# Kernel optimization log

Measured on AMD Instinct MI355X. Metric: run time of the kernel, lower is better.

Reference implementation:

```python
import jax, jax.numpy as jnp
import numpy as np

S = 3072        # packed sequence length
DIM = 1280      # hidden size
H = 16          # num heads
HD = DIM // H   # head dim = 80
NSEG = 3        # number of packed segments


def setup_inputs() -> dict:
    key = jax.random.key(0)
    ks = jax.random.split(key, 6)
    hidden_states = jax.random.normal(ks[0], (S, DIM), jnp.float32)
    cos = jax.random.uniform(ks[1], (S, HD), jnp.float32, minval=-1.0, maxval=1.0)
    sin = jax.random.uniform(ks[2], (S, HD), jnp.float32, minval=-1.0, maxval=1.0)
    qkv_w = jax.random.normal(ks[3], (3 * DIM, DIM), jnp.float32) * 0.02
    qkv_b = jnp.zeros((3 * DIM,), jnp.float32)
    proj_w = jax.random.normal(ks[4], (DIM, DIM), jnp.float32) * 0.02
    proj_b = jnp.zeros((DIM,), jnp.float32)
    # 3 equal segments; cu_seqlens = [0, 1024, 2048, 3072]
    cu_seqlens = jnp.arange(NSEG + 1, dtype=jnp.int32) * (S // NSEG)
    return {
        "hidden_states": hidden_states, "cos": cos, "sin": sin,
        "qkv_w": qkv_w, "qkv_b": qkv_b, "proj_w": proj_w, "proj_b": proj_b,
        "cu_seqlens": cu_seqlens,
    }


def rotate_half(x):
    x1, x2 = jnp.split(x, 2, axis=-1)
    return jnp.concatenate((-x2, x1), axis=-1)


def reference(hidden_states, cos, sin, qkv_w, qkv_b, proj_w, proj_b, cu_seqlens):
    seq = hidden_states.shape[0]
    # QKV projection: [S, 3*DIM] -> [S, 3, H, HD]
    qkv = (hidden_states @ qkv_w.T + qkv_b).reshape(seq, 3, H, HD)
    q, k, v = qkv[:, 0], qkv[:, 1], qkv[:, 2]  # each [S, H, HD]
    # RoPE in float32, cos/sin broadcast over heads via [S, 1, HD]
    c = cos[:, None, :].astype(jnp.float32)
    s = sin[:, None, :].astype(jnp.float32)
    qf, kf = q.astype(jnp.float32), k.astype(jnp.float32)
    q = (qf * c + rotate_half(qf) * s).astype(q.dtype)
    k = (kf * c + rotate_half(kf) * s).astype(k.dtype)
    # Block-diagonal additive mask from cu_seqlens (vectorized, no loop)
    pos = jnp.arange(seq)
    seg = jnp.searchsorted(cu_seqlens, pos, side="right")  # segment id per token
    neg = jnp.finfo(jnp.float32).min
    mask = jnp.where(seg[:, None] == seg[None, :], 0.0, neg)  # [S, S]
    # Dense attention over packed sequence
    scores = jnp.einsum("shd,thd->hst", q, k) / np.sqrt(HD).astype(np.float32)
    scores = scores + mask  # broadcast over heads
    attn = jax.nn.softmax(scores.astype(jnp.float32), axis=-1).astype(q.dtype)
    out = jnp.einsum("hst,thd->shd", attn, v).reshape(seq, DIM)
    return out @ proj_w.T + proj_b
```

## Files before the change

### kernel.cpp

```cpp
#include <hip/hip_runtime.h>
#include <hip/hip_bf16.h>


#define S_TOT 3072
#define DIM   1280
#define NH    16
#define HD    80
#define SEG   1024
#define TDIM  3840

typedef short v8s __attribute__((ext_vector_type(8)));
typedef float v4f __attribute__((ext_vector_type(4)));

__device__ __forceinline__ short f2bf(float v) {
  __hip_bfloat16 b = __float2bfloat16(v);
  return *reinterpret_cast<short*>(&b);
}

__device__ __forceinline__ float bf2f(short s) {
  unsigned u = ((unsigned)(unsigned short)s) << 16;
  float f;
  __builtin_memcpy(&f, &u, 4);
  return f;
}

#define CVT_N1 (S_TOT * DIM / 4)
#define CVT_N2 (TDIM * DIM / 4)
#define CVT_N3 (DIM * DIM / 4)
__global__ __launch_bounds__(256) void cvt3(const float* __restrict__ in1,
                                            const float* __restrict__ in2,
                                            const float* __restrict__ in3,
                                            __hip_bfloat16* __restrict__ o1,
                                            __hip_bfloat16* __restrict__ o2,
                                            __hip_bfloat16* __restrict__ o3) {
  int i = blockIdx.x * 256 + threadIdx.x;
  const float* in;
  __hip_bfloat16* out;
  if (i < CVT_N1) { in = in1; out = o1; }
  else if (i < CVT_N1 + CVT_N2) { in = in2; out = o2; i -= CVT_N1; }
  else { in = in3; out = o3; i -= CVT_N1 + CVT_N2; }
  const float4 v = ((const float4*)in)[i];
  __hip_bfloat162 p0, p1;
  p0.x = __float2bfloat16(v.x); p0.y = __float2bfloat16(v.y);
  p1.x = __float2bfloat16(v.z); p1.y = __float2bfloat16(v.w);
  __hip_bfloat162* o = (__hip_bfloat162*)(out + (size_t)i * 4);
  o[0] = p0; o[1] = p1;
}

__global__ __launch_bounds__(256) void gemm1_c(const __hip_bfloat16* __restrict__ A,
                                               const __hip_bfloat16* __restrict__ B,
                                               const float* __restrict__ bias,
                                               __hip_bfloat16* __restrict__ C,
                                               int M, int N, int K) {
  __shared__ __align__(16) short Abuf[2][8192];
  __shared__ __align__(16) short Bbuf[2][8192];
  const int tid  = threadIdx.x;
  const int wave = tid >> 6;
  const int lane = tid & 63;
  const int quad = lane >> 4;
  const int l16  = lane & 15;
  const int bm = blockIdx.x * 128;
  const int bn = blockIdx.y * 128;
  const int wm = (wave >> 1) * 64;
  const int wn = (wave & 1) * 64;

  const int srow = tid >> 3;
  const int skh  = tid & 7;
  const __hip_bfloat16* Ag[4];
  const __hip_bfloat16* Bg[4];
  int So[4];
  #pragma unroll
  for (int l = 0; l < 4; ++l) {
    const int row = l * 32 + srow;
    Ag[l] = A + (size_t)(bm + row) * K + skh * 8;
    Bg[l] = B + (size_t)(bn + row) * K + skh * 8;
    So[l] = (row * 8 + (skh ^ (row & 7))) * 8;
  }

  v4f acc[4][4];
  const v4f vz = {0.f, 0.f, 0.f, 0.f};
  #pragma unroll
  for (int i = 0; i < 4; ++i)
    #pragma unroll
    for (int j = 0; j < 4; ++j) acc[i][j] = vz;

  const int sw = l16 & 7;
  const int nk = K >> 6;
  v8s ra[4], rb[4];

  #pragma unroll
  for (int l = 0; l < 4; ++l) { ra[l] = *(const v8s*)Ag[l]; rb[l] = *(const v8s*)Bg[l]; }
  #pragma unroll
  for (int l = 0; l < 4; ++l) {
    *(v8s*)&Abuf[0][So[l]] = ra[l];
    *(v8s*)&Bbuf[0][So[l]] = rb[l];
  }
  __syncthreads();

  for (int k = 0; k < nk; ++k) {
    const int cur = k & 1;
    const bool more = (k + 1 < nk);
    if (more) {
      const int off = (k + 1) * 64;
      #pragma unroll
      for (int l = 0; l < 4; ++l) {
        ra[l] = *(const v8s*)(Ag[l] + off);
        rb[l] = *(const v8s*)(Bg[l] + off);
      }
    }
    #pragma unroll
    for (int s = 0; s < 2; ++s) {
      const int khx = (s * 4 + quad) ^ sw;
      v8s af[4], bf[4];
      #pragma unroll
      for (int i = 0; i < 4; ++i) {
        af[i] = *(const v8s*)&Abuf[cur][((wm + i * 16 + l16) * 8 + khx) * 8];
        bf[i] = *(const v8s*)&Bbuf[cur][((wn + i * 16 + l16) * 8 + khx) * 8];
      }
      #pragma unroll
      for (int i = 0; i < 4; ++i)
        #pragma unroll
        for (int j = 0; j < 4; ++j)
          acc[i][j] = __builtin_amdgcn_mfma_f32_16x16x32_bf16(af[i], bf[j], acc[i][j], 0, 0, 0);
    }
    if (more) {
      #pragma unroll
      for (int l = 0; l < 4; ++l) {
        *(v8s*)&Abuf[1 - cur][So[l]] = ra[l];
        *(v8s*)&Bbuf[1 - cur][So[l]] = rb[l];
      }
    }
    __syncthreads();
  }

  #pragma unroll
  for (int j = 0; j < 4; ++j) {
    const int col = bn + wn + j * 16 + l16;
    const float bj = bias[col];
    #pragma unroll
    for (int i = 0; i < 4; ++i) {
      const int row0 = bm + wm + i * 16 + quad * 4;
      #pragma unroll
      for (int r = 0; r < 4; ++r)
        C[(size_t)(row0 + r) * N + col] = __float2bfloat16(acc[i][j][r] + bj);
    }
  }
}

__global__ __launch_bounds__(256) void gemm2_c(const __hip_bfloat16* __restrict__ A,
                                               const __hip_bfloat16* __restrict__ B,
                                               const float* __restrict__ bias,
                                               float* __restrict__ C,
                                               int M, int N, int K) {
  __shared__ __align__(16) short Abuf[2][4096];
  __shared__ __align__(16) short Bbuf[2][8192];
  const int tid  = threadIdx.x;
  const int wave = tid >> 6;
  const int lane = tid & 63;
  const int quad = lane >> 4;
  const int l16  = lane & 15;
  const int bm = blockIdx.x * 64;
  const int bn = blockIdx.y * 128;
  const int wm = (wave & 1) * 32;
  const int wn = (wave >> 1) * 64;

  const int srow = tid >> 3;
  const int skh  = tid & 7;
  const __hip_bfloat16* Ag[2];
  const __hip_bfloat16* Bg[4];
  int Ao[2], Bo[4];
  #pragma unroll
  for (int l = 0; l < 2; ++l) {
    const int row = l * 32 + srow;
    Ag[l] = A + (size_t)(bm + row) * K + skh * 8;
    Ao[l] = (row * 8 + (skh ^ (row & 7))) * 8;
  }
  #pragma unroll
  for (int l = 0; l < 4; ++l) {
    const int row = l * 32 + srow;
    Bg[l] = B + (size_t)(bn + row) * K + skh * 8;
    Bo[l] = (row * 8 + (skh ^ (row & 7))) * 8;
  }

  v4f acc[2][4];
  const v4f vz = {0.f, 0.f, 0.f, 0.f};
  #pragma unroll
  for (int i = 0; i < 2; ++i)
    #pragma unroll
    for (int j = 0; j < 4; ++j) acc[i][j] = vz;

  const int sw = l16 & 7;
  const int nk = K >> 6;
  v8s ra[2], rb[4];

  #pragma unroll
  for (int l = 0; l < 2; ++l) ra[l] = *(const v8s*)Ag[l];
  #pragma unroll
  for (int l = 0; l < 4; ++l) rb[l] = *(const v8s*)Bg[l];
  #pragma unroll
  for (int l = 0; l < 2; ++l) *(v8s*)&Abuf[0][Ao[l]] = ra[l];
  #pragma unroll
  for (int l = 0; l < 4; ++l) *(v8s*)&Bbuf[0][Bo[l]] = rb[l];
  __syncthreads();

  for (int k = 0; k < nk; ++k) {
    const int cur = k & 1;
    const bool more = (k + 1 < nk);
    if (more) {
      const int off = (k + 1) * 64;
      #pragma unroll
      for (int l = 0; l < 2; ++l) ra[l] = *(const v8s*)(Ag[l] + off);
      #pragma unroll
      for (int l = 0; l < 4; ++l) rb[l] = *(const v8s*)(Bg[l] + off);
    }
    #pragma unroll
    for (int s = 0; s < 2; ++s) {
      const int khx = (s * 4 + quad) ^ sw;
      v8s af[2], bf[4];
      #pragma unroll
      for (int i = 0; i < 2; ++i)
        af[i] = *(const v8s*)&Abuf[cur][((wm + i * 16 + l16) * 8 + khx) * 8];
      #pragma unroll
      for (int j = 0; j < 4; ++j)
        bf[j] = *(const v8s*)&Bbuf[cur][((wn + j * 16 + l16) * 8 + khx) * 8];
      #pragma unroll
      for (int i = 0; i < 2; ++i)
        #pragma unroll
        for (int j = 0; j < 4; ++j)
          acc[i][j] = __builtin_amdgcn_mfma_f32_16x16x32_bf16(af[i], bf[j], acc[i][j], 0, 0, 0);
    }
    if (more) {
      #pragma unroll
      for (int l = 0; l < 2; ++l) *(v8s*)&Abuf[1 - cur][Ao[l]] = ra[l];
      #pragma unroll
      for (int l = 0; l < 4; ++l) *(v8s*)&Bbuf[1 - cur][Bo[l]] = rb[l];
    }
    __syncthreads();
  }

  #pragma unroll
  for (int j = 0; j < 4; ++j) {
    const int col = bn + wn + j * 16 + l16;
    const float bj = bias[col];
    #pragma unroll
    for (int i = 0; i < 2; ++i) {
      const int row0 = bm + wm + i * 16 + quad * 4;
      #pragma unroll
      for (int r = 0; r < 4; ++r)
        C[(size_t)(row0 + r) * N + col] = acc[i][j][r] + bj;
    }
  }
}

#define QK_BLOCKS ((2 * S_TOT * 16 * 12) / 256)
#define V_BLOCKS  ((3 * 16 * 16 * 8 * 96) / 256)
__global__ __launch_bounds__(256) void pack_all(const __hip_bfloat16* __restrict__ qkv,
                                                const float* __restrict__ cos_,
                                                const float* __restrict__ sin_,
                                                short* __restrict__ Qp,
                                                short* __restrict__ Kp,
                                                short* __restrict__ Vp) {
  const int bid = blockIdx.x;
  if (bid < QK_BLOCKS) {
    const int idx = bid * 256 + threadIdx.x;
    const int kd = idx % 12;
    const int h  = (idx / 12) % 16;
    const int s  = (idx / 192) % S_TOT;
    const int p  = idx / (192 * S_TOT);
    const int seg = s >> 10, tb = (s >> 6) & 15, t = s & 63;
    short* out = (p ? Kp : Qp) +
                 ((size_t)(((seg * 16 + h) * 16 + tb) * 12 + kd) * 64 + t) * 8;
    short tmp[8];
    if (kd >= 10) {
      #pragma unroll
      for (int j = 0; j < 8; ++j) tmp[j] = 0;
      *(int4*)out = *(int4*)tmp;
      return;
    }
    const short* row = (const short*)qkv + (size_t)s * TDIM + p * DIM + h * HD;
    const int d0 = kd * 8;
    const v8s xm = *(const v8s*)(row + d0);
    const v8s xr = *(const v8s*)(row + d0 + ((kd < 5) ? 40 : -40));
    const float sgn = (kd < 5) ? -1.f : 1.f;
    const float scale = (p == 0) ? 0.111803398874989485f : 1.0f;
    #pragma unroll
    for (int j = 0; j < 8; ++j) {
      const int d = d0 + j;
      const float v = (bf2f(xm[j]) * cos_[s * HD + d] +
                       sgn * bf2f(xr[j]) * sin_[s * HD + d]) * scale;
      tmp[j] = f2bf(v);
    }
    *(int4*)out = *(int4*)tmp;
  } else {
    const int idx = (bid - QK_BLOCKS) * 256 + threadIdx.x;
    const int d  = idx % 96;
    const int td = (idx / 96) % 8;
    const int tb = (idx / 768) % 16;
    const int h  = (idx / (768 * 16)) % 16;
    const int seg = idx / (768 * 256);
    const int s0 = seg * SEG + tb * 64 + td * 8;
    const short* q = (const short*)qkv;
    short tmp[8];
    if (d < 80) {
      #pragma unroll
      for (int j = 0; j < 8; ++j)
        tmp[j] = q[(size_t)(s0 + j) * TDIM + 2 * DIM + h * HD + d];
    } else {
      const short fill = (d == 80) ? (short)0x3F80 : (short)0;
      #pragma unroll
      for (int j = 0; j < 8; ++j) tmp[j] = fill;
    }
    *(int4*)(Vp + (size_t)idx * 8) = *(int4*)tmp;
  }
}

__global__ __launch_bounds__(256, 4) void attn_mfma(const short* __restrict__ Qp,
                                                    const short* __restrict__ Kp,
                                                    const short* __restrict__ Vp,
                                                    __hip_bfloat16* __restrict__ out) {
  __shared__ __align__(16) short Ks[64 * 96];
  __shared__ __align__(16) short Vs[64 * 96];
  __shared__ __align__(16) short Ps[4][16 * 68];

  const int qt  = blockIdx.x;
  const int h   = blockIdx.y;
  const int seg = blockIdx.z;
  const int tid  = threadIdx.x;
  const int wave = tid >> 6;
  const int lane = tid & 63;
  const int quad = lane >> 4;
  const int l16  = lane & 15;
  const int sh16 = seg * 16 + h;

  const short* Qg = Qp + (size_t)(sh16 * 16 + qt) * 6144;
  const short* Kg = Kp + (size_t)sh16 * 16 * 6144;
  const short* Vg = Vp + (size_t)sh16 * 16 * 6144;

  v8s af[3];
  #pragma unroll
  for (int ks = 0; ks < 3; ++ks)
    af[ks] = *(const v8s*)(Qg + ((ks * 4 + quad) * 64 + wave * 16 + l16) * 8);

  v8s kr[3], vr[3];
  #pragma unroll
  for (int it = 0; it < 3; ++it) {
    const int o = (it * 256 + tid) * 8;
    kr[it] = *(const v8s*)(Kg + o);
    vr[it] = *(const v8s*)(Vg + o);
  }
  #pragma unroll
  for (int it = 0; it < 3; ++it) {
    const int o = (it * 256 + tid) * 8;
    *(v8s*)&Ks[o] = kr[it];
    *(v8s*)&Vs[o] = vr[it];
  }
  __syncthreads();

  v4f o4[6];
  const v4f vz = {0.f, 0.f, 0.f, 0.f};
  #pragma unroll
  for (int n = 0; n < 6; ++n) o4[n] = vz;

  for (int kb = 0; kb < 16; ++kb) {
    const bool more = (kb + 1 < 16);
    if (more) {
      const size_t base = (size_t)(kb + 1) * 6144;
      #pragma unroll
      for (int it = 0; it < 3; ++it) {
        const int o = (it * 256 + tid) * 8;
        kr[it] = *(const v8s*)(Kg + base + o);
        vr[it] = *(const v8s*)(Vg + base + o);
      }
    }

    v4f s4[4];
    #pragma unroll
    for (int j = 0; j < 4; ++j) {
      s4[j] = vz;
      #pragma unroll
      for (int ks = 0; ks < 3; ++ks) {
        const v8s bf = *(const v8s*)&Ks[((ks * 4 + quad) * 64 + j * 16 + l16) * 8];
        s4[j] = __builtin_amdgcn_mfma_f32_16x16x32_bf16(af[ks], bf, s4[j], 0, 0, 0);
      }
    }

    #pragma unroll
    for (int reg = 0; reg < 4; ++reg)
      #pragma unroll
      for (int j = 0; j < 4; ++j)
        Ps[wave][(quad * 4 + reg) * 68 + j * 16 + l16] = f2bf(__expf(s4[j][reg]));

    v8s pa[2];
    #pragma unroll
    for (int kp = 0; kp < 2; ++kp)
      pa[kp] = *(const v8s*)&Ps[wave][l16 * 68 + kp * 32 + quad * 8];
    #pragma unroll
    for (int n = 0; n < 6; ++n) {
      #pragma unroll
      for (int kp = 0; kp < 2; ++kp) {
        const v8s vb = *(const v8s*)&Vs[((kp * 4 + quad) * 96 + n * 16 + l16) * 8];
        o4[n] = __builtin_amdgcn_mfma_f32_16x16x32_bf16(pa[kp], vb, o4[n], 0, 0, 0);
      }
    }

    __syncthreads();
    if (more) {
      #pragma unroll
      for (int it = 0; it < 3; ++it) {
        const int o = (it * 256 + tid) * 8;
        *(v8s*)&Ks[o] = kr[it];
        *(v8s*)&Vs[o] = vr[it];
      }
    }
    __syncthreads();
  }

  float inv[4];
  #pragma unroll
  for (int r = 0; r < 4; ++r)
    inv[r] = 1.f / __shfl(o4[5][r], quad << 4);
  const int row0 = seg * SEG + qt * 64 + wave * 16 + quad * 4;
  #pragma unroll
  for (int n = 0; n < 5; ++n) {
    const int col = h * HD + n * 16 + l16;
    #pragma unroll
    for (int r = 0; r < 4; ++r)
      out[(size_t)(row0 + r) * DIM + col] = __float2bfloat16(o4[n][r] * inv[r]);
  }
}

extern "C" void kernel_launch(void* const* d_in, const int* in_sizes, int n_in,
                              void* d_out, int out_size, void* d_ws, size_t ws_size,
                              hipStream_t stream) {
  (void)in_sizes; (void)n_in; (void)out_size; (void)ws_size;
  const float* hs     = (const float*)d_in[0];
  const float* cosp   = (const float*)d_in[1];
  const float* sinp   = (const float*)d_in[2];
  const float* qkv_w  = (const float*)d_in[3];
  const float* qkv_b  = (const float*)d_in[4];
  const float* proj_w = (const float*)d_in[5];
  const float* proj_b = (const float*)d_in[6];

  float* out_f = (float*)d_out;
  __hip_bfloat16* qkv_b16 = (__hip_bfloat16*)d_ws;
  __hip_bfloat16* hs_b    = qkv_b16 + (size_t)S_TOT * TDIM;
  __hip_bfloat16* qkvw_b  = hs_b + (size_t)S_TOT * DIM;
  __hip_bfloat16* projw_b = qkvw_b + (size_t)TDIM * DIM;
  short* Qp = (short*)qkvw_b;
  short* Kp = (short*)(projw_b + (size_t)DIM * DIM);
  short* Vp = Kp + (size_t)3 * 16 * 16 * 6144;
  __hip_bfloat16* attn_b = hs_b;

  cvt3<<<(CVT_N1 + CVT_N2 + CVT_N3) / 256, 256, 0, stream>>>(
      hs, qkv_w, proj_w, hs_b, qkvw_b, projw_b);

  gemm1_c<<<dim3(S_TOT / 128, TDIM / 128), 256, 0, stream>>>(
      hs_b, qkvw_b, qkv_b, qkv_b16, S_TOT, TDIM, DIM);

  pack_all<<<QK_BLOCKS + V_BLOCKS, 256, 0, stream>>>(qkv_b16, cosp, sinp, Qp, Kp, Vp);

  attn_mfma<<<dim3(16, NH, 3), 256, 0, stream>>>(Qp, Kp, Vp, attn_b);

  gemm2_c<<<dim3(S_TOT / 64, DIM / 128), 256, 0, stream>>>(
      attn_b, projw_b, proj_b, out_f, S_TOT, DIM, DIM);
}
```

Baseline: 205.2 us.

## Stage GEMM tiles via direct global-to-LDS loads with pre-swizzled source addresses

Both GEMM kernels (QKV and output projection) now fill their double-buffered LDS tiles with global_load_lds 16-byte transfers instead of loading into registers and then writing to LDS. The XOR swizzle moves from the LDS destination to the global source column, so each wave's contiguous LDS slot receives the right swizzled chunk. This removes the staging registers and the explicit LDS stores, which should lower register pressure and let loads go straight to LDS. It depends on the hardware supporting 16-byte direct LDS loads and on the wave-contiguous destination mapping matching the read-side swizzle.

```diff
diff --git a/kernel.cpp b/kernel.cpp
--- a/kernel.cpp
+++ b/kernel.cpp
@@ -22,6 +22,12 @@
   float f;
   __builtin_memcpy(&f, &u, 4);
   return f;
+}
+
+__device__ __forceinline__ void gload16(const void* g, void* lds) {
+  __builtin_amdgcn_global_load_lds(
+      (const __attribute__((address_space(1))) char*)g,
+      (__attribute__((address_space(3))) char*)lds, 16, 0, 0);
 }
 
 #define CVT_N1 (S_TOT * DIM / 4)
@@ -66,15 +72,16 @@
 
   const int srow = tid >> 3;
   const int skh  = tid & 7;
+  const int khs  = skh ^ (srow & 7);
   const __hip_bfloat16* Ag[4];
   const __hip_bfloat16* Bg[4];
-  int So[4];
+  int Lo[4];
   #pragma unroll
   for (int l = 0; l < 4; ++l) {
     const int row = l * 32 + srow;
-    Ag[l] = A + (size_t)(bm + row) * K + skh * 8;
-    Bg[l] = B + (size_t)(bn + row) * K + skh * 8;
-    So[l] = (row * 8 + (skh ^ (row & 7))) * 8;
+    Ag[l] = A + (size_t)(bm + row) * K + khs * 8;
+    Bg[l] = B + (size_t)(bn + row) * K + khs * 8;
+    Lo[l] = (l * 256 + wave * 64) * 8;
   }
 
   v4f acc[4][4];
@@ -86,26 +93,23 @@
 
   const int sw = l16 & 7;
   const int nk = K >> 6;
-  v8s ra[4], rb[4];
-
-  #pragma unroll
-  for (int l = 0; l < 4; ++l) { ra[l] = *(const v8s*)Ag[l]; rb[l] = *(const v8s*)Bg[l]; }
+
   #pragma unroll
   for (int l = 0; l < 4; ++l) {
-    *(v8s*)&Abuf[0][So[l]] = ra[l];
-    *(v8s*)&Bbuf[0][So[l]] = rb[l];
+    gload16(Ag[l], &Abuf[0][Lo[l]]);
+    gload16(Bg[l], &Bbuf[0][Lo[l]]);
   }
   __syncthreads();
 
   for (int k = 0; k < nk; ++k) {
     const int cur = k & 1;
-    const bool more = (k + 1 < nk);
-    if (more) {
+    if (k + 1 < nk) {
       const int off = (k + 1) * 64;
+      const int nxt = 1 - cur;
       #pragma unroll
       for (int l = 0; l < 4; ++l) {
-        ra[l] = *(const v8s*)(Ag[l] + off);
-        rb[l] = *(const v8s*)(Bg[l] + off);
+        gload16(Ag[l] + off, &Abuf[nxt][Lo[l]]);
+        gload16(Bg[l] + off, &Bbuf[nxt][Lo[l]]);
       }
     }
     #pragma unroll
@@ -122,13 +126,6 @@
         #pragma unroll
         for (int j = 0; j < 4; ++j)
           acc[i][j] = __builtin_amdgcn_mfma_f32_16x16x32_bf16(af[i], bf[j], acc[i][j], 0, 0, 0);
-    }
-    if (more) {
-      #pragma unroll
-      for (int l = 0; l < 4; ++l) {
-        *(v8s*)&Abuf[1 - cur][So[l]] = ra[l];
-        *(v8s*)&Bbuf[1 - cur][So[l]] = rb[l];
-      }
     }
     __syncthreads();
   }
@@ -166,20 +163,21 @@
 
   const int srow = tid >> 3;
   const int skh  = tid & 7;
+  const int khs  = skh ^ (srow & 7);
   const __hip_bfloat16* Ag[2];
   const __hip_bfloat16* Bg[4];
-  int Ao[2], Bo[4];
+  int ALo[2], BLo[4];
   #pragma unroll
   for (int l = 0; l < 2; ++l) {
     const int row = l * 32 + srow;
-    Ag[l] = A + (size_t)(bm + row) * K + skh * 8;
-    Ao[l] = (row * 8 + (skh ^ (row & 7))) * 8;
+    Ag[l] = A + (size_t)(bm + row) * K + khs * 8;
+    ALo[l] = (l * 256 + wave * 64) * 8;
   }
   #pragma unroll
   for (int l = 0; l < 4; ++l) {
     const int row = l * 32 + srow;
-    Bg[l] = B + (size_t)(bn + row) * K + skh * 8;
-    Bo[l] = (row * 8 + (skh ^ (row & 7))) * 8;
+    Bg[l] = B + (size_t)(bn + row) * K + khs * 8;
+    BLo[l] = (l * 256 + wave * 64) * 8;
   }
 
   v4f acc[2][4];
@@ -191,27 +189,22 @@
 
   const int sw = l16 & 7;
   const int nk = K >> 6;
-  v8s ra[2], rb[4];
-
-  #pragma unroll
-  for (int l = 0; l < 2; ++l) ra[l] = *(const v8s*)Ag[l];
-  #pragma unroll
-  for (int l = 0; l < 4; ++l) rb[l] = *(const v8s*)Bg[l];
-  #pragma unroll
-  for (int l = 0; l < 2; ++l) *(v8s*)&Abuf[0][Ao[l]] = ra[l];
-  #pragma unroll
-  for (int l = 0; l < 4; ++l) *(v8s*)&Bbuf[0][Bo[l]] = rb[l];
+
+  #pragma unroll
+  for (int l = 0; l < 2; ++l) gload16(Ag[l], &Abuf[0][ALo[l]]);
+  #pragma unroll
+  for (int l = 0; l < 4; ++l) gload16(Bg[l], &Bbuf[0][BLo[l]]);
   __syncthreads();
 
   for (int k = 0; k < nk; ++k) {
     const int cur = k & 1;
-    const bool more = (k + 1 < nk);
-    if (more) {
+    if (k + 1 < nk) {
       const int off = (k + 1) * 64;
-      #pragma unroll
-      for (int l = 0; l < 2; ++l) ra[l] = *(const v8s*)(Ag[l] + off);
-      #pragma unroll
-      for (int l = 0; l < 4; ++l) rb[l] = *(const v8s*)(Bg[l] + off);
+      const int nxt = 1 - cur;
+      #pragma unroll
+      for (int l = 0; l < 2; ++l) gload16(Ag[l] + off, &Abuf[nxt][ALo[l]]);
+      #pragma unroll
+      for (int l = 0; l < 4; ++l) gload16(Bg[l] + off, &Bbuf[nxt][BLo[l]]);
     }
     #pragma unroll
     for (int s = 0; s < 2; ++s) {
@@ -228,12 +221,6 @@
         #pragma unroll
         for (int j = 0; j < 4; ++j)
           acc[i][j] = __builtin_amdgcn_mfma_f32_16x16x32_bf16(af[i], bf[j], acc[i][j], 0, 0, 0);
-    }
-    if (more) {
-      #pragma unroll
-      for (int l = 0; l < 2; ++l) *(v8s*)&Abuf[1 - cur][Ao[l]] = ra[l];
-      #pragma unroll
-      for (int l = 0; l < 4; ++l) *(v8s*)&Bbuf[1 - cur][Bo[l]] = rb[l];
     }
     __syncthreads();
   }
```

Result: slower. 217.4 us (+5.9%).

## Rewrite QKV GEMM with 256x256 tiles and a 4-stage direct-to-LDS load ring

Applied to the files above, without the earlier changes.

Replaces the double-buffered 128x128 QKV projection GEMM with a 512-thread kernel that computes 256x256 output tiles. Operand tiles go straight from global memory into a 4-deep LDS ring through global_load_lds, gated by vmcnt waits and barriers, so three K-steps of loads are in flight while MFMAs run. The larger tile raises data reuse per load, but the grid shrinks to 180 blocks and 128 KB of dynamic shared memory is needed per block, which may leave some compute units idle and cut occupancy.

```diff
diff --git a/kernel.cpp b/kernel.cpp
--- a/kernel.cpp
+++ b/kernel.cpp
@@ -22,6 +22,12 @@
   float f;
   __builtin_memcpy(&f, &u, 4);
   return f;
+}
+
+__device__ __forceinline__ void gload16(const void* g, void* lds) {
+  __builtin_amdgcn_global_load_lds(
+      (const __attribute__((address_space(1))) char*)g,
+      (__attribute__((address_space(3))) char*)lds, 16, 0, 0);
 }
 
 #define CVT_N1 (S_TOT * DIM / 4)
@@ -47,99 +53,89 @@
   o[0] = p0; o[1] = p1;
 }
 
-__global__ __launch_bounds__(256) void gemm1_c(const __hip_bfloat16* __restrict__ A,
-                                               const __hip_bfloat16* __restrict__ B,
-                                               const float* __restrict__ bias,
-                                               __hip_bfloat16* __restrict__ C,
-                                               int M, int N, int K) {
-  __shared__ __align__(16) short Abuf[2][8192];
-  __shared__ __align__(16) short Bbuf[2][8192];
+extern __shared__ short ring[];
+
+__global__ __launch_bounds__(512, 2) void gemm1_p(const __hip_bfloat16* __restrict__ A,
+                                                  const __hip_bfloat16* __restrict__ B,
+                                                  const float* __restrict__ bias,
+                                                  __hip_bfloat16* __restrict__ C,
+                                                  int M, int N, int K) {
   const int tid  = threadIdx.x;
   const int wave = tid >> 6;
   const int lane = tid & 63;
   const int quad = lane >> 4;
   const int l16  = lane & 15;
-  const int bm = blockIdx.x * 128;
-  const int bn = blockIdx.y * 128;
-  const int wm = (wave >> 1) * 64;
-  const int wn = (wave & 1) * 64;
-
-  const int srow = tid >> 3;
-  const int skh  = tid & 7;
-  const __hip_bfloat16* Ag[4];
-  const __hip_bfloat16* Bg[4];
-  int So[4];
-  #pragma unroll
-  for (int l = 0; l < 4; ++l) {
-    const int row = l * 32 + srow;
-    Ag[l] = A + (size_t)(bm + row) * K + skh * 8;
-    Bg[l] = B + (size_t)(bn + row) * K + skh * 8;
-    So[l] = (row * 8 + (skh ^ (row & 7))) * 8;
-  }
-
-  v4f acc[4][4];
+  const int wmp  = wave >> 2;
+  const int wnp  = wave & 3;
+  const int bm = blockIdx.x * 256;
+  const int bn = blockIdx.y * 256;
+
+  const int srow = tid >> 2;
+  const int sc   = tid & 3;
+  const int kc   = sc ^ (srow & 3);
+  const short* aA0 = (const short*)A + (size_t)(bm + srow) * K + kc * 8;
+  const short* aA1 = aA0 + (size_t)128 * K;
+  const short* bB0 = (const short*)B + (size_t)(bn + srow) * K + kc * 8;
+  const short* bB1 = bB0 + (size_t)128 * K;
+  const int wst = wave * 512;
+
+#define STAGE1(t) do {                                   \
+    short* rb_ = ring + (((t) & 3) * 16384);             \
+    const int ko_ = (t) * 32;                            \
+    gload16(aA0 + ko_, rb_ + wst);                       \
+    gload16(aA1 + ko_, rb_ + 4096 + wst);                \
+    gload16(bB0 + ko_, rb_ + 8192 + wst);                \
+    gload16(bB1 + ko_, rb_ + 12288 + wst);               \
+  } while (0)
+
+  v4f acc[8][4];
   const v4f vz = {0.f, 0.f, 0.f, 0.f};
   #pragma unroll
-  for (int i = 0; i < 4; ++i)
+  for (int i = 0; i < 8; ++i)
     #pragma unroll
     for (int j = 0; j < 4; ++j) acc[i][j] = vz;
 
-  const int sw = l16 & 7;
-  const int nk = K >> 6;
-  v8s ra[4], rb[4];
-
-  #pragma unroll
-  for (int l = 0; l < 4; ++l) { ra[l] = *(const v8s*)Ag[l]; rb[l] = *(const v8s*)Bg[l]; }
-  #pragma unroll
-  for (int l = 0; l < 4; ++l) {
-    *(v8s*)&Abuf[0][So[l]] = ra[l];
-    *(v8s*)&Bbuf[0][So[l]] = rb[l];
-  }
-  __syncthreads();
-
-  for (int k = 0; k < nk; ++k) {
-    const int cur = k & 1;
-    const bool more = (k + 1 < nk);
-    if (more) {
-      const int off = (k + 1) * 64;
-      #pragma unroll
-      for (int l = 0; l < 4; ++l) {
-        ra[l] = *(const v8s*)(Ag[l] + off);
-        rb[l] = *(const v8s*)(Bg[l] + off);
-      }
-    }
-    #pragma unroll
-    for (int s = 0; s < 2; ++s) {
-      const int khx = (s * 4 + quad) ^ sw;
-      v8s af[4], bf[4];
-      #pragma unroll
-      for (int i = 0; i < 4; ++i) {
-        af[i] = *(const v8s*)&Abuf[cur][((wm + i * 16 + l16) * 8 + khx) * 8];
-        bf[i] = *(const v8s*)&Bbuf[cur][((wn + i * 16 + l16) * 8 + khx) * 8];
-      }
-      #pragma unroll
-      for (int i = 0; i < 4; ++i)
-        #pragma unroll
-        for (int j = 0; j < 4; ++j)
-          acc[i][j] = __builtin_amdgcn_mfma_f32_16x16x32_bf16(af[i], bf[j], acc[i][j], 0, 0, 0);
-    }
-    if (more) {
-      #pragma unroll
-      for (int l = 0; l < 4; ++l) {
-        *(v8s*)&Abuf[1 - cur][So[l]] = ra[l];
-        *(v8s*)&Bbuf[1 - cur][So[l]] = rb[l];
-      }
-    }
-    __syncthreads();
-  }
+  const int nt  = K >> 5;
+  const int khx = quad ^ (l16 & 3);
+
+  STAGE1(0); STAGE1(1); STAGE1(2);
+
+  for (int t = 0; t < nt; ++t) {
+    const int rem = nt - 1 - t;
+    if (rem >= 2)      asm volatile("s_waitcnt vmcnt(8)" ::: "memory");
+    else if (rem == 1) asm volatile("s_waitcnt vmcnt(4)" ::: "memory");
+    else               asm volatile("s_waitcnt vmcnt(0)" ::: "memory");
+    __builtin_amdgcn_s_barrier();
+    __builtin_amdgcn_sched_barrier(0);
+
+    const short* rb2 = ring + ((t & 3) * 16384);
+    v8s afr[8], bfr[4];
+    #pragma unroll
+    for (int i = 0; i < 8; ++i)
+      afr[i] = *(const v8s*)&rb2[((wmp * 128 + i * 16 + l16) * 4 + khx) * 8];
+    #pragma unroll
+    for (int j = 0; j < 4; ++j)
+      bfr[j] = *(const v8s*)&rb2[8192 + ((wnp * 64 + j * 16 + l16) * 4 + khx) * 8];
+    #pragma unroll
+    for (int i = 0; i < 8; ++i)
+      #pragma unroll
+      for (int j = 0; j < 4; ++j)
+        acc[i][j] = __builtin_amdgcn_mfma_f32_16x16x32_bf16(afr[i], bfr[j], acc[i][j], 0, 0, 0);
+
+    __builtin_amdgcn_sched_barrier(0);
+    __builtin_amdgcn_s_barrier();
+    __builtin_amdgcn_sched_barrier(0);
+    if (t + 3 < nt) STAGE1(t + 3);
+  }
+#undef STAGE1
 
   #pragma unroll
   for (int j = 0; j < 4; ++j) {
-    const int col = bn + wn + j * 16 + l16;
+    const int col = bn + wnp * 64 + j * 16 + l16;
     const float bj = bias[col];
     #pragma unroll
-    for (int i = 0; i < 4; ++i) {
-      const int row0 = bm + wm + i * 16 + quad * 4;
+    for (int i = 0; i < 8; ++i) {
+      const int row0 = bm + wmp * 128 + i * 16 + quad * 4;
       #pragma unroll
       for (int r = 0; r < 4; ++r)
         C[(size_t)(row0 + r) * N + col] = __float2bfloat16(acc[i][j][r] + bj);
@@ -451,10 +447,17 @@
   short* Vp = Kp + (size_t)3 * 16 * 16 * 6144;
   __hip_bfloat16* attn_b = hs_b;
 
+  static bool attr_set = false;
+  if (!attr_set) {
+    hipFuncSetAttribute((const void*)gemm1_p,
+                        hipFuncAttributeMaxDynamicSharedMemorySize, 131072);
+    attr_set = true;
+  }
+
   cvt3<<<(CVT_N1 + CVT_N2 + CVT_N3) / 256, 256, 0, stream>>>(
       hs, qkv_w, proj_w, hs_b, qkvw_b, projw_b);
 
-  gemm1_c<<<dim3(S_TOT / 128, TDIM / 128), 256, 0, stream>>>(
+  gemm1_p<<<dim3(S_TOT / 256, TDIM / 256), 512, 131072, stream>>>(
       hs_b, qkvw_b, qkv_b, qkv_b16, S_TOT, TDIM, DIM);
 
   pack_all<<<QK_BLOCKS + V_BLOCKS, 256, 0, stream>>>(qkv_b16, cosp, sinp, Qp, Kp, Vp);
```

New measurement: 215.4 us. 1.05x slower.
